# Performance work log

Measured on AMD Instinct MI355X. Metric: run time of the kernel, lower is better.

The kernel has to match this reference:

```python
import jax, jax.numpy as jnp
import numpy as np

T = 0.04
PIC_NUM = 4  # images per identity (hardcoded in SP_loss)


def setup_inputs() -> dict:
    key = jax.random.key(0)
    N, D = 8192, 256  # 2048 identities x 4 images, 256-dim ReID features
    x = jax.random.normal(key, (N, D), dtype=jnp.float32)
    x = x / jnp.linalg.norm(x, axis=1, keepdims=True)  # L2-normalize (cosine sims)
    return {"x": x}


def reference(x):
    N = x.shape[0]
    G = N // PIC_NUM  # number of identity groups
    s = (x @ x.T) / T  # [N, N] scaled similarity matrix

    # Diagonal 4x4 blocks: within-class similarities. [G, 4, 4]
    d4 = s.reshape(G, PIC_NUM, G, PIC_NUM)
    gidx = jnp.arange(G)
    pos = d4[gidx, :, gidx, :]  # [G, 4, 4]

    # hard positive: -T * log( sum_{i,j in class} exp(-dot_ij / T) )  (soft-min)
    hard_pos = -T * jax.nn.logsumexp(-pos.reshape(G, PIC_NUM * PIC_NUM), axis=1)

    # least-hard positive: T * log( sum_i 1 / (sum_j exp(-dot_ij / T)) )
    lse_row = jax.nn.logsumexp(-pos, axis=2)           # [G, 4] = log sum_j exp(-dot/T)
    least_pos = T * jax.nn.logsumexp(-lse_row, axis=1)  # [G]

    # negatives: T * log( sum_{i in class, j not in class} exp(dot_ij / T) )
    col_group = jnp.arange(N) // PIC_NUM              # [N]
    same = col_group[None, :] == gidx[:, None]        # [G, N] same-class column mask
    s3 = s.reshape(G, PIC_NUM, N)
    neg_masked = jnp.where(same[:, None, :], -jnp.inf, s3)
    neg = T * jax.nn.logsumexp(neg_masked.reshape(G, PIC_NUM * N), axis=1)  # [G]

    # Original detaches all three S vectors before forming the loss.
    hard_pos = jax.lax.stop_gradient(hard_pos)
    least_pos = jax.lax.stop_gradient(least_pos)
    neg = jax.lax.stop_gradient(neg)

    # alpha: harmonic mean of (hard, least-hard) when hard >= 0, else 0
    alpha = jnp.where(hard_pos >= 0.0,
                      2.0 * least_pos * hard_pos / (hard_pos + least_pos),
                      0.0)
    margin = alpha * hard_pos + (1.0 - alpha) * least_pos
    # log(1 + exp(z)) == softplus(z), numerically stable, same math
    loss = jnp.mean(jax.nn.softplus((neg - margin) / T))
    return loss
```

## Files before the change

### kernel.cpp

```cpp
#include <hip/hip_runtime.h>
#include <math.h>


#define NROWS 8192
#define DDIM  256
#define NGRP  2048
#define NTB   64
#define NTILES (NTB * (NTB + 1) / 2)
#define T_CONST 0.04f
#define INV_T   25.0f
#define EXP2_SCALE 36.06737602222409f
#define SCALE_QTR 0x7B7B7B7Bu

typedef __attribute__((ext_vector_type(8))) int   i32x8_t;
typedef __attribute__((ext_vector_type(4))) int   i32x4_t;
typedef __attribute__((ext_vector_type(4))) float f32x4_t;

typedef const __attribute__((address_space(1))) void gv_t;
typedef __attribute__((address_space(3))) void lv_t;

__device__ __forceinline__ void gll16(const void* g, void* l) {
    __builtin_amdgcn_global_load_lds((gv_t*)g, (lv_t*)l, 16, 0, 0);
}

__global__ __launch_bounds__(256) void prep_kernel(const float* __restrict__ x,
                                                   unsigned int* __restrict__ xq,
                                                   float* __restrict__ rowsum,
                                                   float* __restrict__ margin) {
    const int b = blockIdx.x;
    if (b < 2048) {
        int gid = b * 256 + threadIdx.x;
        float4 v = *(const float4*)(x + gid * 4);
        int pk = __builtin_amdgcn_cvt_pk_fp8_f32(v.x * 16.f, v.y * 16.f, 0, false);
        pk = __builtin_amdgcn_cvt_pk_fp8_f32(v.z * 16.f, v.w * 16.f, pk, true);
        xq[gid] = (unsigned int)pk;
        if (gid < NROWS) rowsum[gid] = 0.f;
        return;
    }
    const int g = (b - 2048) * 4 + (threadIdx.x >> 6);
    const int lane = threadIdx.x & 63;
    const float* xr = x + (size_t)g * 4 * DDIM;
    float a[16];
#pragma unroll
    for (int k = 0; k < 16; ++k) a[k] = 0.f;
    for (int e = lane; e < DDIM; e += 64) {
        float vv[4];
        vv[0] = xr[e];
        vv[1] = xr[DDIM + e];
        vv[2] = xr[2 * DDIM + e];
        vv[3] = xr[3 * DDIM + e];
#pragma unroll
        for (int i = 0; i < 4; ++i)
#pragma unroll
            for (int j = 0; j < 4; ++j)
                a[i * 4 + j] = fmaf(vv[i], vv[j], a[i * 4 + j]);
    }
#pragma unroll
    for (int k = 0; k < 16; ++k) {
        float t = a[k];
        t += __shfl_xor(t, 32, 64);
        t += __shfl_xor(t, 16, 64);
        t += __shfl_xor(t, 8, 64);
        t += __shfl_xor(t, 4, 64);
        t += __shfl_xor(t, 2, 64);
        t += __shfl_xor(t, 1, 64);
        a[k] = t;
    }
    if (lane == 0) {
        float pos[16];
#pragma unroll
        for (int k = 0; k < 16; ++k) pos[k] = a[k] * INV_T;

        float mx = -pos[0];
#pragma unroll
        for (int k = 1; k < 16; ++k) mx = fmaxf(mx, -pos[k]);
        float se = 0.f;
#pragma unroll
        for (int k = 0; k < 16; ++k) se += __expf(-pos[k] - mx);
        float hard_pos = -T_CONST * (mx + __logf(se));

        float lse_row[4];
#pragma unroll
        for (int i = 0; i < 4; ++i) {
            float m2 = -pos[i * 4];
#pragma unroll
            for (int j = 1; j < 4; ++j) m2 = fmaxf(m2, -pos[i * 4 + j]);
            float s2 = 0.f;
#pragma unroll
            for (int j = 0; j < 4; ++j) s2 += __expf(-pos[i * 4 + j] - m2);
            lse_row[i] = m2 + __logf(s2);
        }
        float m3 = -lse_row[0];
#pragma unroll
        for (int i = 1; i < 4; ++i) m3 = fmaxf(m3, -lse_row[i]);
        float s3 = 0.f;
#pragma unroll
        for (int i = 0; i < 4; ++i) s3 += __expf(-lse_row[i] - m3);
        float least_pos = T_CONST * (m3 + __logf(s3));

        float alpha = (hard_pos >= 0.f)
                          ? (2.f * least_pos * hard_pos) / (hard_pos + least_pos)
                          : 0.f;
        margin[g] = alpha * hard_pos + (1.f - alpha) * least_pos;
    }
}

__global__ __launch_bounds__(256) void gemm_exp_rowsum(const unsigned char* __restrict__ xq,
                                                       float* __restrict__ rowsum) {
    __shared__ unsigned char Als[128 * 128];
    __shared__ unsigned char Bls[128 * 128];
    __shared__ float rowacc[128];
    __shared__ float colacc[128];

    const int idx = blockIdx.x;
    int bi = (int)((129.0f - sqrtf(16641.0f - 8.0f * (float)idx)) * 0.5f);
    while (bi * (129 - bi) / 2 > idx) --bi;
    while ((bi + 1) * (128 - bi) / 2 <= idx) ++bi;
    const int bj = bi + (idx - bi * (129 - bi) / 2);
    const int row0 = bi * 128;
    const int col0 = bj * 128;
    const bool diag = (bi == bj);

    const int tid = threadIdx.x;
    const int lane = tid & 63;
    const int w = tid >> 6;
    const int wrow = (w >> 1) * 64;
    const int wcol = (w & 1) * 64;
    const int quad = lane >> 4;
    const int l16 = lane & 15;
    const int p = tid & 7;

    if (tid < 128) { rowacc[tid] = 0.f; colacc[tid] = 0.f; }

    f32x4_t acc[4][4];
#pragma unroll
    for (int i = 0; i < 4; ++i)
#pragma unroll
        for (int j = 0; j < 4; ++j)
            acc[i][j] = (f32x4_t){0.f, 0.f, 0.f, 0.f};

#pragma unroll
    for (int ks = 0; ks < 2; ++ks) {
        if (ks) __syncthreads();
#pragma unroll
        for (int i = 0; i < 4; ++i) {
            const int gi = i * 256 + tid;
            const int srow = gi >> 3;
            const int g = p ^ (srow & 7);
            gll16(xq + ((size_t)(row0 + srow) << 8) + ks * 128 + g * 16, &Als[gi * 16]);
        }
#pragma unroll
        for (int i = 0; i < 4; ++i) {
            const int gi = i * 256 + tid;
            const int srow = gi >> 3;
            const int g = p ^ (srow & 7);
            gll16(xq + ((size_t)(col0 + srow) << 8) + ks * 128 + g * 16, &Bls[gi * 16]);
        }
        __syncthreads();

        i32x8_t aF[4], bF[4];
#pragma unroll
        for (int mi = 0; mi < 4; ++mi) {
            const int m = wrow + mi * 16 + l16;
            const int base = m * 128;
            i32x4_t lo = *(const i32x4_t*)&Als[base + (((2 * quad) ^ (m & 7)) << 4)];
            i32x4_t hi = *(const i32x4_t*)&Als[base + (((2 * quad + 1) ^ (m & 7)) << 4)];
            aF[mi] = __builtin_shufflevector(lo, hi, 0, 1, 2, 3, 4, 5, 6, 7);
        }
#pragma unroll
        for (int ni = 0; ni < 4; ++ni) {
            const int n = wcol + ni * 16 + l16;
            const int base = n * 128;
            i32x4_t lo = *(const i32x4_t*)&Bls[base + (((2 * quad) ^ (n & 7)) << 4)];
            i32x4_t hi = *(const i32x4_t*)&Bls[base + (((2 * quad + 1) ^ (n & 7)) << 4)];
            bF[ni] = __builtin_shufflevector(lo, hi, 0, 1, 2, 3, 4, 5, 6, 7);
        }
#pragma unroll
        for (int mi = 0; mi < 4; ++mi)
#pragma unroll
            for (int ni = 0; ni < 4; ++ni)
                acc[mi][ni] = __builtin_amdgcn_mfma_scale_f32_16x16x128_f8f6f4(
                    aF[mi], bF[ni], acc[mi][ni],
                    0, 0,
                    0, (int)SCALE_QTR,
                    0, (int)SCALE_QTR);
    }

    if (!diag) {
        float colv[4] = {0.f, 0.f, 0.f, 0.f};
#pragma unroll
        for (int mi = 0; mi < 4; ++mi) {
#pragma unroll
            for (int reg = 0; reg < 4; ++reg) {
                const int lrow = wrow + mi * 16 + quad * 4 + reg;
                float rv = 0.f;
#pragma unroll
                for (int ni = 0; ni < 4; ++ni) {
                    float e = exp2f(acc[mi][ni][reg] * EXP2_SCALE);
                    rv += e;
                    colv[ni] += e;
                }
                rv += __shfl_xor(rv, 1, 64);
                rv += __shfl_xor(rv, 2, 64);
                rv += __shfl_xor(rv, 4, 64);
                rv += __shfl_xor(rv, 8, 64);
                if (l16 == 0) atomicAdd(&rowacc[lrow], rv);
            }
        }
#pragma unroll
        for (int ni = 0; ni < 4; ++ni) {
            float cv = colv[ni];
            cv += __shfl_xor(cv, 16, 64);
            cv += __shfl_xor(cv, 32, 64);
            if (quad == 0) atomicAdd(&colacc[wcol + ni * 16 + l16], cv);
        }
    } else {
#pragma unroll
        for (int mi = 0; mi < 4; ++mi) {
#pragma unroll
            for (int reg = 0; reg < 4; ++reg) {
                const int lrow = wrow + mi * 16 + quad * 4 + reg;
                const int grp = (row0 + lrow) >> 2;
                float rv = 0.f;
#pragma unroll
                for (int ni = 0; ni < 4; ++ni) {
                    const int gcol = col0 + wcol + ni * 16 + l16;
                    rv += ((gcol >> 2) == grp) ? 0.f : exp2f(acc[mi][ni][reg] * EXP2_SCALE);
                }
                rv += __shfl_xor(rv, 1, 64);
                rv += __shfl_xor(rv, 2, 64);
                rv += __shfl_xor(rv, 4, 64);
                rv += __shfl_xor(rv, 8, 64);
                if (l16 == 0) atomicAdd(&rowacc[lrow], rv);
            }
        }
    }
    __syncthreads();
    if (tid < 128) {
        atomicAdd(&rowsum[row0 + tid], rowacc[tid]);
        if (!diag) atomicAdd(&rowsum[col0 + tid], colacc[tid]);
    }
}

__global__ __launch_bounds__(256) void finalize_kernel(const float* __restrict__ rowsum,
                                                       const float* __restrict__ margin,
                                                       float* __restrict__ out) {
    const int tid = threadIdx.x;
    float local = 0.f;
    for (int g = tid; g < NGRP; g += 256) {
        float s = rowsum[4 * g] + rowsum[4 * g + 1] + rowsum[4 * g + 2] + rowsum[4 * g + 3];
        float z = __logf(s) - margin[g] * INV_T;
        float sp = (z > 30.f) ? z : log1pf(__expf(z));
        local += sp;
    }
    local += __shfl_xor(local, 1, 64);
    local += __shfl_xor(local, 2, 64);
    local += __shfl_xor(local, 4, 64);
    local += __shfl_xor(local, 8, 64);
    local += __shfl_xor(local, 16, 64);
    local += __shfl_xor(local, 32, 64);
    __shared__ float wsum[4];
    if ((tid & 63) == 0) wsum[tid >> 6] = local;
    __syncthreads();
    if (tid == 0) out[0] = (wsum[0] + wsum[1] + wsum[2] + wsum[3]) * (1.f / (float)NGRP);
}

extern "C" void kernel_launch(void* const* d_in, const int* in_sizes, int n_in,
                              void* d_out, int out_size, void* d_ws, size_t ws_size,
                              hipStream_t stream) {
    const float* x = (const float*)d_in[0];
    float* out = (float*)d_out;

    unsigned int* xq = (unsigned int*)d_ws;
    float* rowsum = (float*)((char*)d_ws + (size_t)NROWS * DDIM);
    float* margin = rowsum + NROWS;

    prep_kernel<<<2048 + 512, 256, 0, stream>>>(x, xq, rowsum, margin);
    gemm_exp_rowsum<<<NTILES, 256, 0, stream>>>((const unsigned char*)xq, rowsum);
    finalize_kernel<<<1, 256, 0, stream>>>(rowsum, margin, out);
}
```

Before: 110.1 us.

## Use single-wave 64x64 tiles with direct global fragment loads and group sums

Replaces the 256-thread 128x128 block tile staged through LDS with a single-wavefront 64x64 tile that loads MFMA fragments straight from global memory (L2), with no shared memory or barriers. Row and column exp-sums are now reduced per identity group in registers and atomically added to a group-level sum array, so the finalize kernel no longer combines four row sums. The aim is to drop LDS staging, block syncs and shared atomics and to raise occupancy. In exchange there are four times as many tiles, operand reuse within a block falls, so global/L2 traffic rises, and there are more global atomics.

```diff
diff --git a/kernel.cpp b/kernel.cpp
--- a/kernel.cpp
+++ b/kernel.cpp
@@ -5,7 +5,7 @@
 #define NROWS 8192
 #define DDIM  256
 #define NGRP  2048
-#define NTB   64
+#define NTB   128
 #define NTILES (NTB * (NTB + 1) / 2)
 #define T_CONST 0.04f
 #define INV_T   25.0f
@@ -16,16 +16,9 @@
 typedef __attribute__((ext_vector_type(4))) int   i32x4_t;
 typedef __attribute__((ext_vector_type(4))) float f32x4_t;
 
-typedef const __attribute__((address_space(1))) void gv_t;
-typedef __attribute__((address_space(3))) void lv_t;
-
-__device__ __forceinline__ void gll16(const void* g, void* l) {
-    __builtin_amdgcn_global_load_lds((gv_t*)g, (lv_t*)l, 16, 0, 0);
-}
-
 __global__ __launch_bounds__(256) void prep_kernel(const float* __restrict__ x,
                                                    unsigned int* __restrict__ xq,
-                                                   float* __restrict__ rowsum,
+                                                   float* __restrict__ grpsum,
                                                    float* __restrict__ margin) {
     const int b = blockIdx.x;
     if (b < 2048) {
@@ -34,7 +27,7 @@
         int pk = __builtin_amdgcn_cvt_pk_fp8_f32(v.x * 16.f, v.y * 16.f, 0, false);
         pk = __builtin_amdgcn_cvt_pk_fp8_f32(v.z * 16.f, v.w * 16.f, pk, true);
         xq[gid] = (unsigned int)pk;
-        if (gid < NROWS) rowsum[gid] = 0.f;
+        if (gid < NGRP) grpsum[gid] = 0.f;
         return;
     }
     const int g = (b - 2048) * 4 + (threadIdx.x >> 6);
@@ -105,32 +98,20 @@
     }
 }
 
-__global__ __launch_bounds__(256) void gemm_exp_rowsum(const unsigned char* __restrict__ xq,
-                                                       float* __restrict__ rowsum) {
-    __shared__ unsigned char Als[128 * 128];
-    __shared__ unsigned char Bls[128 * 128];
-    __shared__ float rowacc[128];
-    __shared__ float colacc[128];
-
+__global__ __launch_bounds__(64, 3) void gemm_exp_grpsum(const unsigned char* __restrict__ xq,
+                                                         float* __restrict__ grpsum) {
     const int idx = blockIdx.x;
-    int bi = (int)((129.0f - sqrtf(16641.0f - 8.0f * (float)idx)) * 0.5f);
-    while (bi * (129 - bi) / 2 > idx) --bi;
-    while ((bi + 1) * (128 - bi) / 2 <= idx) ++bi;
-    const int bj = bi + (idx - bi * (129 - bi) / 2);
-    const int row0 = bi * 128;
-    const int col0 = bj * 128;
-    const bool diag = (bi == bj);
-
-    const int tid = threadIdx.x;
-    const int lane = tid & 63;
-    const int w = tid >> 6;
-    const int wrow = (w >> 1) * 64;
-    const int wcol = (w & 1) * 64;
+    int ti = (int)((257.0f - sqrtf(66049.0f - 8.0f * (float)idx)) * 0.5f);
+    while (ti * (257 - ti) / 2 > idx) --ti;
+    while ((ti + 1) * (256 - ti) / 2 <= idx) ++ti;
+    const int tj = ti + (idx - ti * (257 - ti) / 2);
+    const int row0 = ti * 64;
+    const int col0 = tj * 64;
+    const bool diag = (ti == tj);
+
+    const int lane = threadIdx.x;
     const int quad = lane >> 4;
     const int l16 = lane & 15;
-    const int p = tid & 7;
-
-    if (tid < 128) { rowacc[tid] = 0.f; colacc[tid] = 0.f; }
 
     f32x4_t acc[4][4];
 #pragma unroll
@@ -141,38 +122,21 @@
 
 #pragma unroll
     for (int ks = 0; ks < 2; ++ks) {
-        if (ks) __syncthreads();
-#pragma unroll
-        for (int i = 0; i < 4; ++i) {
-            const int gi = i * 256 + tid;
-            const int srow = gi >> 3;
-            const int g = p ^ (srow & 7);
-            gll16(xq + ((size_t)(row0 + srow) << 8) + ks * 128 + g * 16, &Als[gi * 16]);
-        }
-#pragma unroll
-        for (int i = 0; i < 4; ++i) {
-            const int gi = i * 256 + tid;
-            const int srow = gi >> 3;
-            const int g = p ^ (srow & 7);
-            gll16(xq + ((size_t)(col0 + srow) << 8) + ks * 128 + g * 16, &Bls[gi * 16]);
-        }
-        __syncthreads();
-
         i32x8_t aF[4], bF[4];
 #pragma unroll
         for (int mi = 0; mi < 4; ++mi) {
-            const int m = wrow + mi * 16 + l16;
-            const int base = m * 128;
-            i32x4_t lo = *(const i32x4_t*)&Als[base + (((2 * quad) ^ (m & 7)) << 4)];
-            i32x4_t hi = *(const i32x4_t*)&Als[base + (((2 * quad + 1) ^ (m & 7)) << 4)];
+            const unsigned char* pa =
+                xq + ((size_t)(row0 + mi * 16 + l16) << 8) + ks * 128 + quad * 32;
+            i32x4_t lo = *(const i32x4_t*)pa;
+            i32x4_t hi = *(const i32x4_t*)(pa + 16);
             aF[mi] = __builtin_shufflevector(lo, hi, 0, 1, 2, 3, 4, 5, 6, 7);
         }
 #pragma unroll
         for (int ni = 0; ni < 4; ++ni) {
-            const int n = wcol + ni * 16 + l16;
-            const int base = n * 128;
-            i32x4_t lo = *(const i32x4_t*)&Bls[base + (((2 * quad) ^ (n & 7)) << 4)];
-            i32x4_t hi = *(const i32x4_t*)&Bls[base + (((2 * quad + 1) ^ (n & 7)) << 4)];
+            const unsigned char* pb =
+                xq + ((size_t)(col0 + ni * 16 + l16) << 8) + ks * 128 + quad * 32;
+            i32x4_t lo = *(const i32x4_t*)pb;
+            i32x4_t hi = *(const i32x4_t*)(pb + 16);
             bF[ni] = __builtin_shufflevector(lo, hi, 0, 1, 2, 3, 4, 5, 6, 7);
         }
 #pragma unroll
@@ -186,70 +150,68 @@
                     0, (int)SCALE_QTR);
     }
 
+    const int rg0 = row0 >> 2;
+    const int cg0 = col0 >> 2;
+    float rowg[4] = {0.f, 0.f, 0.f, 0.f};
+    float colp[4] = {0.f, 0.f, 0.f, 0.f};
+
     if (!diag) {
-        float colv[4] = {0.f, 0.f, 0.f, 0.f};
-#pragma unroll
-        for (int mi = 0; mi < 4; ++mi) {
-#pragma unroll
-            for (int reg = 0; reg < 4; ++reg) {
-                const int lrow = wrow + mi * 16 + quad * 4 + reg;
-                float rv = 0.f;
+#pragma unroll
+        for (int mi = 0; mi < 4; ++mi)
+#pragma unroll
+            for (int reg = 0; reg < 4; ++reg)
 #pragma unroll
                 for (int ni = 0; ni < 4; ++ni) {
                     float e = exp2f(acc[mi][ni][reg] * EXP2_SCALE);
-                    rv += e;
-                    colv[ni] += e;
+                    rowg[mi] += e;
+                    colp[ni] += e;
                 }
-                rv += __shfl_xor(rv, 1, 64);
-                rv += __shfl_xor(rv, 2, 64);
-                rv += __shfl_xor(rv, 4, 64);
-                rv += __shfl_xor(rv, 8, 64);
-                if (l16 == 0) atomicAdd(&rowacc[lrow], rv);
-            }
-        }
+    } else {
+#pragma unroll
+        for (int mi = 0; mi < 4; ++mi) {
+            const int rgrp = mi * 4 + quad;
+#pragma unroll
+            for (int reg = 0; reg < 4; ++reg)
+#pragma unroll
+                for (int ni = 0; ni < 4; ++ni) {
+                    const int cgrp = ni * 4 + (l16 >> 2);
+                    float e = (cgrp == rgrp) ? 0.f
+                                             : exp2f(acc[mi][ni][reg] * EXP2_SCALE);
+                    rowg[mi] += e;
+                }
+        }
+    }
+
+#pragma unroll
+    for (int mi = 0; mi < 4; ++mi) {
+        float v = rowg[mi];
+        v += __shfl_xor(v, 1, 64);
+        v += __shfl_xor(v, 2, 64);
+        v += __shfl_xor(v, 4, 64);
+        v += __shfl_xor(v, 8, 64);
+        if (l16 == 0) atomicAdd(&grpsum[rg0 + mi * 4 + quad], v);
+    }
+    if (!diag) {
 #pragma unroll
         for (int ni = 0; ni < 4; ++ni) {
-            float cv = colv[ni];
-            cv += __shfl_xor(cv, 16, 64);
-            cv += __shfl_xor(cv, 32, 64);
-            if (quad == 0) atomicAdd(&colacc[wcol + ni * 16 + l16], cv);
-        }
-    } else {
-#pragma unroll
-        for (int mi = 0; mi < 4; ++mi) {
-#pragma unroll
-            for (int reg = 0; reg < 4; ++reg) {
-                const int lrow = wrow + mi * 16 + quad * 4 + reg;
-                const int grp = (row0 + lrow) >> 2;
-                float rv = 0.f;
-#pragma unroll
-                for (int ni = 0; ni < 4; ++ni) {
-                    const int gcol = col0 + wcol + ni * 16 + l16;
-                    rv += ((gcol >> 2) == grp) ? 0.f : exp2f(acc[mi][ni][reg] * EXP2_SCALE);
-                }
-                rv += __shfl_xor(rv, 1, 64);
-                rv += __shfl_xor(rv, 2, 64);
-                rv += __shfl_xor(rv, 4, 64);
-                rv += __shfl_xor(rv, 8, 64);
-                if (l16 == 0) atomicAdd(&rowacc[lrow], rv);
-            }
-        }
-    }
-    __syncthreads();
-    if (tid < 128) {
-        atomicAdd(&rowsum[row0 + tid], rowacc[tid]);
-        if (!diag) atomicAdd(&rowsum[col0 + tid], colacc[tid]);
-    }
-}
-
-__global__ __launch_bounds__(256) void finalize_kernel(const float* __restrict__ rowsum,
+            float v = colp[ni];
+            v += __shfl_xor(v, 16, 64);
+            v += __shfl_xor(v, 32, 64);
+            v += __shfl_xor(v, 1, 64);
+            v += __shfl_xor(v, 2, 64);
+            if (quad == 0 && (l16 & 3) == 0)
+                atomicAdd(&grpsum[cg0 + ni * 4 + (l16 >> 2)], v);
+        }
+    }
+}
+
+__global__ __launch_bounds__(256) void finalize_kernel(const float* __restrict__ grpsum,
                                                        const float* __restrict__ margin,
                                                        float* __restrict__ out) {
     const int tid = threadIdx.x;
     float local = 0.f;
     for (int g = tid; g < NGRP; g += 256) {
-        float s = rowsum[4 * g] + rowsum[4 * g + 1] + rowsum[4 * g + 2] + rowsum[4 * g + 3];
-        float z = __logf(s) - margin[g] * INV_T;
+        float z = __logf(grpsum[g]) - margin[g] * INV_T;
         float sp = (z > 30.f) ? z : log1pf(__expf(z));
         local += sp;
     }
@@ -272,10 +234,10 @@
     float* out = (float*)d_out;
 
     unsigned int* xq = (unsigned int*)d_ws;
-    float* rowsum = (float*)((char*)d_ws + (size_t)NROWS * DDIM);
-    float* margin = rowsum + NROWS;
-
-    prep_kernel<<<2048 + 512, 256, 0, stream>>>(x, xq, rowsum, margin);
-    gemm_exp_rowsum<<<NTILES, 256, 0, stream>>>((const unsigned char*)xq, rowsum);
-    finalize_kernel<<<1, 256, 0, stream>>>(rowsum, margin, out);
-}
+    float* grpsum = (float*)((char*)d_ws + (size_t)NROWS * DDIM);
+    float* margin = grpsum + NGRP;
+
+    prep_kernel<<<2048 + 512, 256, 0, stream>>>(x, xq, grpsum, margin);
+    gemm_exp_grpsum<<<NTILES, 64, 0, stream>>>((const unsigned char*)xq, grpsum);
+    finalize_kernel<<<1, 256, 0, stream>>>(grpsum, margin, out);
+}
```

Result: slower. 129.4 us (+17.5%).
